# Performance work log

Hardware: AMD Instinct MI355X
Metric: run time of the kernel (lower is better)

## Reference

```python
import jax, jax.numpy as jnp
import numpy as np

N_NODES = 50000
N_EDGES = 400000
IN_DIM = 512
HID = 512
HID2 = HID // 2
OUT_DIM = 2
NUM_GRAPHS = 500


def setup_inputs() -> dict:
    key = jax.random.key(0)
    ks = jax.random.split(key, 12)
    x = jax.random.normal(ks[0], (N_NODES, IN_DIM), dtype=jnp.float32)
    edge_index = jax.random.randint(ks[1], (2, N_EDGES), 0, N_NODES, dtype=jnp.int64)
    batch = jnp.sort(jax.random.randint(ks[2], (N_NODES,), 0, NUM_GRAPHS, dtype=jnp.int64))
    def lin(k, fan_out, fan_in):
        bound = 1.0 / np.sqrt(fan_in)
        return jax.random.uniform(k, (fan_out, fan_in), jnp.float32, -bound, bound)
    # SAGEConv layer 1: lin_l (on aggregated neighbors, with bias) + lin_r (root)
    W1l = lin(ks[3], HID, IN_DIM)
    b1 = jax.random.uniform(ks[4], (HID,), jnp.float32, -1/np.sqrt(IN_DIM), 1/np.sqrt(IN_DIM))
    W1r = lin(ks[5], HID, IN_DIM)
    # SAGEConv layer 2
    W2l = lin(ks[6], HID2, HID)
    b2 = jax.random.uniform(ks[7], (HID2,), jnp.float32, -1/np.sqrt(HID), 1/np.sqrt(HID))
    W2r = lin(ks[8], HID2, HID)
    # final fc
    Wfc = lin(ks[9], OUT_DIM, HID2)
    bfc = jax.random.uniform(ks[10], (OUT_DIM,), jnp.float32, -1/np.sqrt(HID2), 1/np.sqrt(HID2))
    return {"x": x, "edge_index": edge_index, "batch": batch,
            "W1l": W1l, "b1": b1, "W1r": W1r,
            "W2l": W2l, "b2": b2, "W2r": W2r,
            "Wfc": Wfc, "bfc": bfc}


def _sage_conv(h, src, dst, Wl, bl, Wr):
    # mean-aggregate source features into target nodes, then linear + root term
    n = h.shape[0]
    agg = jax.ops.segment_sum(h[src], dst, num_segments=n)          # [N, d_in]
    deg = jax.ops.segment_sum(jnp.ones(src.shape, h.dtype), dst, num_segments=n)
    agg = agg / jnp.maximum(deg, 1.0)[:, None]
    return agg @ Wl.T + bl + h @ Wr.T


def reference(x, edge_index, batch, W1l, b1, W1r, W2l, b2, W2r, Wfc, bfc):
    src, dst = edge_index[0], edge_index[1]
    h = jax.nn.relu(_sage_conv(x, src, dst, W1l, b1, W1r))
    h = jax.nn.relu(_sage_conv(h, src, dst, W2l, b2, W2r))
    # global mean pool over graph ids
    pooled = jax.ops.segment_sum(h, batch, num_segments=NUM_GRAPHS)  # [G, HID2]
    counts = jax.ops.segment_sum(jnp.ones(batch.shape, h.dtype), batch, num_segments=NUM_GRAPHS)
    pooled = pooled / jnp.maximum(counts, 1.0)[:, None]
    logits = pooled @ Wfc.T + bfc
    return jax.nn.log_softmax(logits, axis=1)
```

## Files before the change

### kernel.cpp

```cpp
#include <hip/hip_runtime.h>
#include <cstdint>

#define N_NODES 50000
#define N_PAD 50048
#define N_EDGES 400000
#define IN_DIM 512
#define HID 512
#define HID2 256
#define NUM_GRAPHS 500
#define SCAN_BLOCKS 196

typedef unsigned short u16;
typedef short s8v __attribute__((ext_vector_type(8)));
typedef float f4v __attribute__((ext_vector_type(4)));
typedef u16 u16x8 __attribute__((ext_vector_type(8)));

__device__ __forceinline__ u16 f2bf(float f) {
  union { float f; uint32_t u; } c;
  c.f = f;
  const uint32_t u = c.u;
  return (u16)((u + 0x7fffu + ((u >> 16) & 1u)) >> 16);
}
__device__ __forceinline__ float bf2f(u16 v) {
  union { uint32_t u; float f; } c;
  c.u = ((uint32_t)v) << 16;
  return c.f;
}

__device__ __forceinline__ void gload16(const void* g, void* l) {
  __builtin_amdgcn_global_load_lds(
      (const __attribute__((address_space(1))) void*)(uintptr_t)g,
      (__attribute__((address_space(3))) void*)(uint32_t)(uintptr_t)l, 16, 0, 0);
}

__global__ __launch_bounds__(256) void cvt_f32_bf16(const float* __restrict__ in,
                                                    u16* __restrict__ out, int n8) {
  const int i = blockIdx.x * 256 + threadIdx.x;
  if (i >= n8) return;
  const float4 a = ((const float4*)in)[2 * i];
  const float4 b = ((const float4*)in)[2 * i + 1];
  u16x8 o;
  o[0] = f2bf(a.x); o[1] = f2bf(a.y); o[2] = f2bf(a.z); o[3] = f2bf(a.w);
  o[4] = f2bf(b.x); o[5] = f2bf(b.y); o[6] = f2bf(b.z); o[7] = f2bf(b.w);
  ((u16x8*)out)[i] = o;
}

__global__ __launch_bounds__(256) void cvt_weights(const float* __restrict__ W1l,
                                                   const float* __restrict__ W1r,
                                                   const float* __restrict__ W2l,
                                                   const float* __restrict__ W2r,
                                                   u16* __restrict__ Wc1,
                                                   u16* __restrict__ Wc2) {
  const int i = blockIdx.x * 256 + threadIdx.x;
  const float* src;
  u16* dstp;
  int l;
  if (i < 32768)      { src = W1l; dstp = Wc1;          l = i; }
  else if (i < 65536) { src = W1r; dstp = Wc1 + 262144; l = i - 32768; }
  else if (i < 81920) { src = W2l; dstp = Wc2;          l = i - 65536; }
  else                { src = W2r; dstp = Wc2 + 131072; l = i - 81920; }
  const float4 a = ((const float4*)src)[2 * l];
  const float4 b = ((const float4*)src)[2 * l + 1];
  u16x8 o;
  o[0] = f2bf(a.x); o[1] = f2bf(a.y); o[2] = f2bf(a.z); o[3] = f2bf(a.w);
  o[4] = f2bf(b.x); o[5] = f2bf(b.y); o[6] = f2bf(b.z); o[7] = f2bf(b.w);
  ((u16x8*)dstp)[l] = o;
}

__global__ __launch_bounds__(256) void gemm_mfma(const u16* __restrict__ A,
                                                 const u16* __restrict__ B,
                                                 u16* __restrict__ C,
                                                 int K, int ldc) {
  __shared__ __align__(16) u16 As[128 * 32];
  __shared__ __align__(16) u16 Bs[128 * 32];
  const int tid = threadIdx.x;
  const int lane = tid & 63;
  const int wave = tid >> 6;
  const int wr = (wave >> 1) * 64;
  const int wc = (wave & 1) * 64;
  const int fr = lane & 15;
  const int fq = lane >> 4;
  const size_t bm = (size_t)blockIdx.x * 128;
  const size_t bn = (size_t)blockIdx.y * 128;

  const int r0 = tid >> 2;
  const int c0 = (tid & 3) * 8;
  const u16* gA = A + (bm + r0) * K + c0;
  const u16* gB = B + (bn + r0) * K + c0;
  u16* lA = As + r0 * 32 + c0;
  u16* lB = Bs + r0 * 32 + c0;
  const size_t rstep = (size_t)64 * K;

  f4v acc[4][4];
#pragma unroll
  for (int m = 0; m < 4; ++m)
#pragma unroll
    for (int n = 0; n < 4; ++n)
      acc[m][n] = f4v{0.f, 0.f, 0.f, 0.f};

  for (int k0 = 0; k0 < K; k0 += 32) {
    __syncthreads();
    gload16(gA + k0, lA);
    gload16(gA + rstep + k0, lA + 64 * 32);
    gload16(gB + k0, lB);
    gload16(gB + rstep + k0, lB + 64 * 32);
    __syncthreads();
    s8v af[4], bf_[4];
#pragma unroll
    for (int m = 0; m < 4; ++m)
      af[m] = *(const s8v*)(As + (wr + m * 16 + fr) * 32 + fq * 8);
#pragma unroll
    for (int n = 0; n < 4; ++n)
      bf_[n] = *(const s8v*)(Bs + (wc + n * 16 + fr) * 32 + fq * 8);
#pragma unroll
    for (int m = 0; m < 4; ++m)
#pragma unroll
      for (int n = 0; n < 4; ++n)
        acc[m][n] = __builtin_amdgcn_mfma_f32_16x16x32_bf16(af[m], bf_[n],
                                                            acc[m][n], 0, 0, 0);
  }

#pragma unroll
  for (int m = 0; m < 4; ++m) {
    const size_t row0 = bm + wr + m * 16 + fq * 4;
#pragma unroll
    for (int n = 0; n < 4; ++n) {
      const size_t col = bn + wc + n * 16 + fr;
#pragma unroll
      for (int i = 0; i < 4; ++i)
        C[(row0 + i) * ldc + col] = f2bf(acc[m][n][i]);
    }
  }
}

__global__ void deg_hist(const int* __restrict__ dst, int* __restrict__ degi, int nE) {
  const int e = blockIdx.x * 256 + threadIdx.x;
  if (e < nE) atomicAdd(&degi[dst[e]], 1);
}

__device__ __forceinline__ int block_scan_excl(int v, int* total_out) {
  const int lane = threadIdx.x & 63;
  const int wid = threadIdx.x >> 6;
  int s = v;
#pragma unroll
  for (int off = 1; off < 64; off <<= 1) {
    const int t = __shfl_up(s, off);
    if (lane >= off) s += t;
  }
  __shared__ int wsum[4];
  if (lane == 63) wsum[wid] = s;
  __syncthreads();
  int base = 0;
#pragma unroll
  for (int w = 0; w < 4; ++w)
    if (w < wid) base += wsum[w];
  *total_out = wsum[0] + wsum[1] + wsum[2] + wsum[3];
  return base + s - v;
}

__global__ __launch_bounds__(256) void scan_blocks(const int* __restrict__ degi,
                                                   int* __restrict__ offs,
                                                   int* __restrict__ bsum, int n) {
  const int gid = blockIdx.x * 256 + threadIdx.x;
  const int v = (gid < n) ? degi[gid] : 0;
  int total;
  const int excl = block_scan_excl(v, &total);
  if (gid < n) offs[gid] = excl;
  if (threadIdx.x == 0) bsum[blockIdx.x] = total;
}

__global__ __launch_bounds__(256) void scan_bsums(int* __restrict__ bsum, int nb) {
  const int v = (threadIdx.x < nb) ? bsum[threadIdx.x] : 0;
  int total;
  const int excl = block_scan_excl(v, &total);
  if (threadIdx.x < nb) bsum[threadIdx.x] = excl;
}

__global__ __launch_bounds__(256) void add_base(int* __restrict__ offs,
                                                const int* __restrict__ bsum,
                                                int n, int nE) {
  const int gid = blockIdx.x * 256 + threadIdx.x;
  if (gid < n) offs[gid] += bsum[blockIdx.x];
  if (gid == 0) offs[n] = nE;
}

__global__ void fill_csr(const int* __restrict__ src, const int* __restrict__ dst,
                         const int* __restrict__ offs, int* __restrict__ cursor,
                         int* __restrict__ sorted_src, int nE) {
  const int e = blockIdx.x * 256 + threadIdx.x;
  if (e < nE) {
    const int d = dst[e];
    const int pos = offs[d] + atomicAdd(&cursor[d], 1);
    sorted_src[pos] = src[e];
  }
}

template <int D, int OUTF32>
__global__ __launch_bounds__(256) void gather_combine(
    const u16* __restrict__ t, const u16* __restrict__ r, int ldt,
    const float* __restrict__ bias, const int* __restrict__ offs,
    const int* __restrict__ ssrc, void* __restrict__ hout) {
  constexpr int LPN = D / 8;
  const int node = (int)((blockIdx.x * 256u + threadIdx.x) / LPN);
  if (node >= N_NODES) return;
  const int o = (int)(threadIdx.x % LPN) * 8;
  const int beg = offs[node], end = offs[node + 1];
  float a[8] = {0.f, 0.f, 0.f, 0.f, 0.f, 0.f, 0.f, 0.f};
  int e = beg;
  for (; e + 3 < end; e += 4) {
    const int s0 = ssrc[e], s1 = ssrc[e + 1], s2 = ssrc[e + 2], s3 = ssrc[e + 3];
    const u16x8 v0 = *(const u16x8*)(t + (size_t)s0 * ldt + o);
    const u16x8 v1 = *(const u16x8*)(t + (size_t)s1 * ldt + o);
    const u16x8 v2 = *(const u16x8*)(t + (size_t)s2 * ldt + o);
    const u16x8 v3 = *(const u16x8*)(t + (size_t)s3 * ldt + o);
#pragma unroll
    for (int j = 0; j < 8; ++j)
      a[j] += (bf2f(v0[j]) + bf2f(v1[j])) + (bf2f(v2[j]) + bf2f(v3[j]));
  }
  for (; e < end; ++e) {
    const u16x8 v0 = *(const u16x8*)(t + (size_t)ssrc[e] * ldt + o);
#pragma unroll
    for (int j = 0; j < 8; ++j) a[j] += bf2f(v0[j]);
  }
  const float invd = 1.0f / fmaxf((float)(end - beg), 1.0f);
  const u16x8 rv = *(const u16x8*)(r + (size_t)node * ldt + o);
  float hv[8];
#pragma unroll
  for (int j = 0; j < 8; ++j)
    hv[j] = fmaxf(fmaf(a[j], invd, bias[o + j] + bf2f(rv[j])), 0.f);
  if (OUTF32) {
    float* hp = (float*)hout + (size_t)node * D + o;
    *(float4*)hp = make_float4(hv[0], hv[1], hv[2], hv[3]);
    *(float4*)(hp + 4) = make_float4(hv[4], hv[5], hv[6], hv[7]);
  } else {
    u16x8 ov;
#pragma unroll
    for (int j = 0; j < 8; ++j) ov[j] = f2bf(hv[j]);
    *(u16x8*)((u16*)hout + (size_t)node * D + o) = ov;
  }
}

__global__ __launch_bounds__(256) void pool_final(const float* __restrict__ h,
                                                  const int* __restrict__ batch,
                                                  const float* __restrict__ Wfc,
                                                  const float* __restrict__ bfc,
                                                  float* __restrict__ out, int nNodes) {
  const int g = blockIdx.x;
  __shared__ int sbeg, send;
  if (threadIdx.x == 0) {
    int lo = 0, hi = nNodes;
    while (lo < hi) { const int mid = (lo + hi) >> 1; if (batch[mid] < g) lo = mid + 1; else hi = mid; }
    sbeg = lo;
    hi = nNodes;
    while (lo < hi) { const int mid = (lo + hi) >> 1; if (batch[mid] < g + 1) lo = mid + 1; else hi = mid; }
    send = lo;
  }
  __syncthreads();
  const int t = threadIdx.x;
  float s = 0.f;
  for (int row = sbeg; row < send; ++row) s += h[(size_t)row * HID2 + t];
  const float cnt = fmaxf((float)(send - sbeg), 1.0f);
  const float p = s / cnt;
  float d0 = p * Wfc[t];
  float d1 = p * Wfc[HID2 + t];
#pragma unroll
  for (int off = 32; off > 0; off >>= 1) {
    d0 += __shfl_down(d0, off);
    d1 += __shfl_down(d1, off);
  }
  __shared__ float r0[4], r1[4];
  const int wid = t >> 6, lane = t & 63;
  if (lane == 0) { r0[wid] = d0; r1[wid] = d1; }
  __syncthreads();
  if (t == 0) {
    const float l0 = r0[0] + r0[1] + r0[2] + r0[3] + bfc[0];
    const float l1 = r1[0] + r1[1] + r1[2] + r1[3] + bfc[1];
    const float m = fmaxf(l0, l1);
    const float lse = m + logf(expf(l0 - m) + expf(l1 - m));
    out[g * 2 + 0] = l0 - lse;
    out[g * 2 + 1] = l1 - lse;
  }
}

extern "C" void kernel_launch(void* const* d_in, const int* in_sizes, int n_in,
                              void* d_out, int out_size, void* d_ws, size_t ws_size,
                              hipStream_t stream) {
  (void)in_sizes; (void)n_in; (void)out_size; (void)ws_size;
  const float* x   = (const float*)d_in[0];
  const int* eidx  = (const int*)d_in[1];
  const int* batch = (const int*)d_in[2];
  const float* W1l = (const float*)d_in[3];
  const float* b1  = (const float*)d_in[4];
  const float* W1r = (const float*)d_in[5];
  const float* W2l = (const float*)d_in[6];
  const float* b2  = (const float*)d_in[7];
  const float* W2r = (const float*)d_in[8];
  const float* Wfc = (const float*)d_in[9];
  const float* bfc = (const float*)d_in[10];
  float* out = (float*)d_out;
  const int* src = eidx;
  const int* dst = eidx + N_EDGES;

  char* ws = (char*)d_ws;
  size_t off = 0;
  auto alloc = [&](size_t bytes) {
    char* p = ws + off;
    off += (bytes + 255) & ~(size_t)255;
    return p;
  };
  u16* C1   = (u16*)alloc((size_t)N_PAD * 1024 * 2);
  u16* bufX = (u16*)alloc((size_t)N_PAD * 512 * 2);
  u16* h1   = (u16*)alloc((size_t)N_PAD * 512 * 2);
  u16* Wc1  = (u16*)alloc((size_t)1024 * 512 * 2);
  u16* Wc2  = (u16*)alloc((size_t)512 * 512 * 2);
  int* degi       = (int*)alloc((size_t)N_NODES * 4);
  int* offs       = (int*)alloc((size_t)(N_NODES + 1) * 4);
  int* cursor     = (int*)alloc((size_t)N_NODES * 4);
  int* sorted_src = (int*)alloc((size_t)N_EDGES * 4);
  int* bsum       = (int*)alloc((size_t)SCAN_BLOCKS * 4);
  u16* C2 = C1;
  float* h2 = (float*)bufX;

  hipMemsetAsync(degi, 0, (size_t)N_NODES * 4, stream);
  hipMemsetAsync(cursor, 0, (size_t)N_NODES * 4, stream);
  deg_hist<<<(N_EDGES + 255) / 256, 256, 0, stream>>>(dst, degi, N_EDGES);
  scan_blocks<<<SCAN_BLOCKS, 256, 0, stream>>>(degi, offs, bsum, N_NODES);
  scan_bsums<<<1, 256, 0, stream>>>(bsum, SCAN_BLOCKS);
  add_base<<<SCAN_BLOCKS, 256, 0, stream>>>(offs, bsum, N_NODES, N_EDGES);
  fill_csr<<<(N_EDGES + 255) / 256, 256, 0, stream>>>(src, dst, offs, cursor,
                                                      sorted_src, N_EDGES);

  cvt_f32_bf16<<<(N_NODES * (IN_DIM / 8) + 255) / 256, 256, 0, stream>>>(
      x, bufX, N_NODES * (IN_DIM / 8));
  cvt_weights<<<384, 256, 0, stream>>>(W1l, W1r, W2l, W2r, Wc1, Wc2);

  {
    dim3 grid(N_PAD / 128, 1024 / 128);
    gemm_mfma<<<grid, 256, 0, stream>>>(bufX, Wc1, C1, IN_DIM, 1024);
  }
  gather_combine<HID, 0><<<(N_NODES + 3) / 4, 256, 0, stream>>>(
      C1, C1 + 512, 1024, b1, offs, sorted_src, h1);

  {
    dim3 grid(N_PAD / 128, 512 / 128);
    gemm_mfma<<<grid, 256, 0, stream>>>(h1, Wc2, C2, HID, 512);
  }
  gather_combine<HID2, 1><<<(N_NODES + 7) / 8, 256, 0, stream>>>(
      C2, C2 + 256, 512, b2, offs, sorted_src, h2);

  pool_final<<<NUM_GRAPHS, 256, 0, stream>>>(h2, batch, Wfc, bfc, out, N_NODES);
}
```

Baseline: 373.9 us.

## Split GEMM output into separate neighbor/root buffers and swizzle blocks across XCDs

The GEMM now writes the lin_l and lin_r halves of its output into two separate dense buffers instead of one interleaved wide matrix. The gather kernel therefore reads compact rows of D elements, which improves locality of the random neighbor gathers. The GEMM also moves to a 1D grid, iterating N-tiles fastest within each row block, with an XCD-aware block-index swizzle so neighboring tiles that share A rows land on the same chiplet's L2. This adds index arithmetic and a second workspace buffer.

```diff
diff --git a/kernel.cpp b/kernel.cpp
--- a/kernel.cpp
+++ b/kernel.cpp
@@ -31,6 +31,12 @@
   __builtin_amdgcn_global_load_lds(
       (const __attribute__((address_space(1))) void*)(uintptr_t)g,
       (__attribute__((address_space(3))) void*)(uint32_t)(uintptr_t)l, 16, 0, 0);
+}
+
+__device__ __forceinline__ int xcd_swizzle(int orig, int nwg) {
+  const int q = nwg >> 3, rr = nwg & 7;
+  const int xcd = orig & 7, idx = orig >> 3;
+  return (xcd < rr ? xcd * (q + 1) : rr * (q + 1) + (xcd - rr) * q) + idx;
 }
 
 __global__ __launch_bounds__(256) void cvt_f32_bf16(const float* __restrict__ in,
@@ -69,10 +75,15 @@
 
 __global__ __launch_bounds__(256) void gemm_mfma(const u16* __restrict__ A,
                                                  const u16* __restrict__ B,
-                                                 u16* __restrict__ C,
-                                                 int K, int ldc) {
+                                                 u16* __restrict__ CT,
+                                                 u16* __restrict__ CR,
+                                                 int K, int nxLog2, int nxHalf,
+                                                 int nwg) {
   __shared__ __align__(16) u16 As[128 * 32];
   __shared__ __align__(16) u16 Bs[128 * 32];
+  const int id = xcd_swizzle(blockIdx.x, nwg);
+  const int bx = id & ((1 << nxLog2) - 1);
+  const int by = id >> nxLog2;
   const int tid = threadIdx.x;
   const int lane = tid & 63;
   const int wave = tid >> 6;
@@ -80,8 +91,8 @@
   const int wc = (wave & 1) * 64;
   const int fr = lane & 15;
   const int fq = lane >> 4;
-  const size_t bm = (size_t)blockIdx.x * 128;
-  const size_t bn = (size_t)blockIdx.y * 128;
+  const size_t bm = (size_t)by * 128;
+  const size_t bn = (size_t)bx * 128;
 
   const int r0 = tid >> 2;
   const int c0 = (tid & 3) * 8;
@@ -120,15 +131,18 @@
                                                             acc[m][n], 0, 0, 0);
   }
 
+  u16* Cb = (bx < nxHalf) ? CT : CR;
+  const int ldc = nxHalf * 128;
+  const size_t cn0 = (size_t)(bx - (bx >= nxHalf ? nxHalf : 0)) * 128 + wc;
 #pragma unroll
   for (int m = 0; m < 4; ++m) {
     const size_t row0 = bm + wr + m * 16 + fq * 4;
 #pragma unroll
     for (int n = 0; n < 4; ++n) {
-      const size_t col = bn + wc + n * 16 + fr;
+      const size_t col = cn0 + n * 16 + fr;
 #pragma unroll
       for (int i = 0; i < 4; ++i)
-        C[(row0 + i) * ldc + col] = f2bf(acc[m][n][i]);
+        Cb[(row0 + i) * ldc + col] = f2bf(acc[m][n][i]);
     }
   }
 }
@@ -197,7 +211,7 @@
 
 template <int D, int OUTF32>
 __global__ __launch_bounds__(256) void gather_combine(
-    const u16* __restrict__ t, const u16* __restrict__ r, int ldt,
+    const u16* __restrict__ t, const u16* __restrict__ r,
     const float* __restrict__ bias, const int* __restrict__ offs,
     const int* __restrict__ ssrc, void* __restrict__ hout) {
   constexpr int LPN = D / 8;
@@ -209,21 +223,21 @@
   int e = beg;
   for (; e + 3 < end; e += 4) {
     const int s0 = ssrc[e], s1 = ssrc[e + 1], s2 = ssrc[e + 2], s3 = ssrc[e + 3];
-    const u16x8 v0 = *(const u16x8*)(t + (size_t)s0 * ldt + o);
-    const u16x8 v1 = *(const u16x8*)(t + (size_t)s1 * ldt + o);
-    const u16x8 v2 = *(const u16x8*)(t + (size_t)s2 * ldt + o);
-    const u16x8 v3 = *(const u16x8*)(t + (size_t)s3 * ldt + o);
+    const u16x8 v0 = *(const u16x8*)(t + (size_t)s0 * D + o);
+    const u16x8 v1 = *(const u16x8*)(t + (size_t)s1 * D + o);
+    const u16x8 v2 = *(const u16x8*)(t + (size_t)s2 * D + o);
+    const u16x8 v3 = *(const u16x8*)(t + (size_t)s3 * D + o);
 #pragma unroll
     for (int j = 0; j < 8; ++j)
       a[j] += (bf2f(v0[j]) + bf2f(v1[j])) + (bf2f(v2[j]) + bf2f(v3[j]));
   }
   for (; e < end; ++e) {
-    const u16x8 v0 = *(const u16x8*)(t + (size_t)ssrc[e] * ldt + o);
+    const u16x8 v0 = *(const u16x8*)(t + (size_t)ssrc[e] * D + o);
 #pragma unroll
     for (int j = 0; j < 8; ++j) a[j] += bf2f(v0[j]);
   }
   const float invd = 1.0f / fmaxf((float)(end - beg), 1.0f);
-  const u16x8 rv = *(const u16x8*)(r + (size_t)node * ldt + o);
+  const u16x8 rv = *(const u16x8*)(r + (size_t)node * D + o);
   float hv[8];
 #pragma unroll
   for (int j = 0; j < 8; ++j)
@@ -308,7 +322,8 @@
     off += (bytes + 255) & ~(size_t)255;
     return p;
   };
-  u16* C1   = (u16*)alloc((size_t)N_PAD * 1024 * 2);
+  u16* bufT = (u16*)alloc((size_t)N_PAD * 512 * 2);
+  u16* bufR = (u16*)alloc((size_t)N_PAD * 512 * 2);
   u16* bufX = (u16*)alloc((size_t)N_PAD * 512 * 2);
   u16* h1   = (u16*)alloc((size_t)N_PAD * 512 * 2);
   u16* Wc1  = (u16*)alloc((size_t)1024 * 512 * 2);
@@ -318,7 +333,6 @@
   int* cursor     = (int*)alloc((size_t)N_NODES * 4);
   int* sorted_src = (int*)alloc((size_t)N_EDGES * 4);
   int* bsum       = (int*)alloc((size_t)SCAN_BLOCKS * 4);
-  u16* C2 = C1;
   float* h2 = (float*)bufX;
 
   hipMemsetAsync(degi, 0, (size_t)N_NODES * 4, stream);
@@ -335,18 +349,18 @@
   cvt_weights<<<384, 256, 0, stream>>>(W1l, W1r, W2l, W2r, Wc1, Wc2);
 
   {
-    dim3 grid(N_PAD / 128, 1024 / 128);
-    gemm_mfma<<<grid, 256, 0, stream>>>(bufX, Wc1, C1, IN_DIM, 1024);
+    const int nwg = (N_PAD / 128) * 8;
+    gemm_mfma<<<nwg, 256, 0, stream>>>(bufX, Wc1, bufT, bufR, IN_DIM, 3, 4, nwg);
   }
   gather_combine<HID, 0><<<(N_NODES + 3) / 4, 256, 0, stream>>>(
-      C1, C1 + 512, 1024, b1, offs, sorted_src, h1);
+      bufT, bufR, b1, offs, sorted_src, h1);
 
   {
-    dim3 grid(N_PAD / 128, 512 / 128);
-    gemm_mfma<<<grid, 256, 0, stream>>>(h1, Wc2, C2, HID, 512);
+    const int nwg = (N_PAD / 128) * 4;
+    gemm_mfma<<<nwg, 256, 0, stream>>>(h1, Wc2, bufT, bufR, HID, 2, 2, nwg);
   }
   gather_combine<HID2, 1><<<(N_NODES + 7) / 8, 256, 0, stream>>>(
-      C2, C2 + 256, 512, b2, offs, sorted_src, h2);
+      bufT, bufR, b2, offs, sorted_src, h2);
 
   pool_final<<<NUM_GRAPHS, 256, 0, stream>>>(h2, batch, Wfc, bfc, out, N_NODES);
 }
```

Result: faster. 359.1 us (-4.0%).
